# Optimization experiments

Hardware: AMD Instinct MI355X
Metric: run time of the kernel (lower is better)

Reference implementation:

```python
import jax, jax.numpy as jnp
import numpy as np

NUM_HEADS = 16
THETA = 10000.0


def apply_rope(x, pos, theta):
    # x: [B, H, S, d], pos: [S] int
    d = x.shape[-1]
    inv_freq = theta ** (-jnp.arange(0, d, 2, dtype=jnp.float32) / d)  # [d/2]
    ang = pos.astype(jnp.float32)[:, None] * inv_freq  # [S, d/2]
    cos, sin = jnp.cos(ang), jnp.sin(ang)
    x1, x2 = x[..., 0::2], x[..., 1::2]
    out_even = x1 * cos - x2 * sin
    out_odd = x1 * sin + x2 * cos
    return jnp.stack([out_even, out_odd], axis=-1).reshape(x.shape)


def setup_inputs() -> dict:
    key = jax.random.key(0)
    ks = jax.random.split(key, 5)
    B, S, D = 4, 2048, 2048
    s = 1.0 / np.sqrt(D)
    return {
        "x": jax.random.normal(ks[0], (B, S, D), dtype=jnp.float32),
        "token_positions": jnp.arange(S, dtype=jnp.int32),
        "wq": jax.random.normal(ks[1], (D, D), dtype=jnp.float32) * s,
        "wk": jax.random.normal(ks[2], (D, D), dtype=jnp.float32) * s,
        "wv": jax.random.normal(ks[3], (D, D), dtype=jnp.float32) * s,
        "wo": jax.random.normal(ks[4], (D, D), dtype=jnp.float32) * s,
    }


def reference(x, token_positions, wq, wk, wv, wo):
    B, S, _ = x.shape
    H = NUM_HEADS
    dh = wq.shape[0] // H

    def proj(w):
        y = jnp.einsum('bsd,ed->bse', x, w)  # Linear: x @ W^T
        return y.reshape(B, S, H, dh).transpose(0, 2, 1, 3)  # [B,H,S,dh]

    Q, K, V = proj(wq), proj(wk), proj(wv)
    Q = apply_rope(Q, token_positions, THETA)
    K = apply_rope(K, token_positions, THETA)

    scores = jnp.einsum('bhqd,bhkd->bhqk', Q, K) / jnp.sqrt(jnp.float32(dh))
    causal = jnp.tril(jnp.ones((S, S), dtype=bool))
    scores = jnp.where(causal, scores, jnp.finfo(scores.dtype).min)
    attn = jax.nn.softmax(scores, axis=-1)
    out = jnp.einsum('bhqk,bhkd->bhqd', attn, V)
    out = out.transpose(0, 2, 1, 3).reshape(B, S, H * dh)
    return jnp.einsum('bsd,ed->bse', out, wo)
```

## Files before the change

kernel.cpp:

```cpp
#include <hip/hip_runtime.h>
#include <math.h>

typedef __bf16 bf16;
typedef bf16 bf16x8 __attribute__((ext_vector_type(8)));
typedef bf16 bf16x4v __attribute__((ext_vector_type(4)));
typedef float f32x4 __attribute__((ext_vector_type(4)));

#define BB 4
#define SS 2048
#define DD 2048
#define HH 16
#define DH 128

__device__ __forceinline__ void gload_lds16(const bf16* g, bf16* l) {
  __builtin_amdgcn_global_load_lds(
      (const __attribute__((address_space(1))) void*)g,
      (__attribute__((address_space(3))) void*)l, 16, 0, 0);
}

__global__ __launch_bounds__(256) void cast_kernel(const float* __restrict__ in,
                                                   bf16* __restrict__ out, int n4) {
  int i = blockIdx.x * blockDim.x + threadIdx.x;
  if (i < n4) {
    const float4 v = ((const float4*)in)[i];
    bf16x4v o = {(bf16)v.x, (bf16)v.y, (bf16)v.z, (bf16)v.w};
    ((bf16x4v*)out)[i] = o;
  }
}

__global__ __launch_bounds__(256) void cast4_kernel(const float* __restrict__ w0,
                                                    const float* __restrict__ w1,
                                                    const float* __restrict__ w2,
                                                    const float* __restrict__ w3,
                                                    bf16* __restrict__ out) {
  const int i = blockIdx.x * blockDim.x + threadIdx.x;
  const int per = (DD * DD) / 4;
  const int sel = i / per, off = i - sel * per;
  const float* src = (sel == 0) ? w0 : (sel == 1) ? w1 : (sel == 2) ? w2 : w3;
  const float4 v = ((const float4*)src)[off];
  bf16x4v o = {(bf16)v.x, (bf16)v.y, (bf16)v.z, (bf16)v.w};
  ((bf16x4v*)(out + (size_t)sel * DD * DD))[off] = o;
}

template <int MODE>
__global__ __launch_bounds__(512, 2) void gemm256(const bf16* __restrict__ A,
                                                  const bf16* __restrict__ Bw,
                                                  bf16* __restrict__ Cb,
                                                  float* __restrict__ Cf,
                                                  const int* __restrict__ pos,
                                                  int M, int N, int K) {
  __shared__ alignas(16) bf16 lds[4][2][256 * 32];

  const int tid = threadIdx.x;
  const int wave = tid >> 6, lane = tid & 63;
  const int quad = lane >> 4, l15 = lane & 15;
  const int wm = wave >> 2, wn = wave & 3;

  const int lin = blockIdx.y * gridDim.x + blockIdx.x;
  const int swz = (lin & 7) * 32 + (lin >> 3);
  const int m0 = (swz >> 3) * 256, n0 = (swz & 7) * 256;

  auto stage = [&](int buf, int ab, const bf16* src, int rbase, int u) {
    bf16* dst = &lds[buf][ab][0];
#pragma unroll
    for (int j = 0; j < 2; ++j) {
      const int c = wave * 128 + j * 64 + lane;
      const int row = c >> 2;
      const int k8 = (c & 3) ^ ((row >> 1) & 3);
      gload_lds16(src + (size_t)(rbase + row) * K + u * 32 + k8 * 8,
                  dst + (size_t)(wave * 128 + j * 64) * 8);
    }
  };

  auto rdA = [&](int buf, int mf) -> bf16x8 {
    const int row = wm * 128 + mf * 16 + l15;
    return *(const bf16x8*)(&lds[buf][0][0] + row * 32 + ((quad ^ ((row >> 1) & 3)) * 8));
  };
  auto rdB = [&](int buf, int nf) -> bf16x8 {
    const int row = wn * 64 + nf * 16 + l15;
    return *(const bf16x8*)(&lds[buf][1][0] + row * 32 + ((quad ^ ((row >> 1) & 3)) * 8));
  };

  f32x4 acc[8][4] = {};
  const int NT = K >> 5;

  stage(0, 0, A, m0, 0);
  stage(0, 1, Bw, n0, 0);
  stage(1, 0, A, m0, 1);
  stage(1, 1, Bw, n0, 1);
  asm volatile("s_waitcnt vmcnt(4)" ::: "memory");
  __builtin_amdgcn_s_barrier();
  __builtin_amdgcn_sched_barrier(0);

  bf16x8 af[4], bfr[4];
  for (int t = 0; t < NT; ++t) {
    const int buf = t & 3;
    const bool pre = (t + 2 < NT);
#pragma unroll
    for (int mf = 0; mf < 4; ++mf) af[mf] = rdA(buf, mf);
#pragma unroll
    for (int nf = 0; nf < 4; ++nf) bfr[nf] = rdB(buf, nf);
    if (pre) stage((t + 2) & 3, 0, A, m0, t + 2);
    __builtin_amdgcn_sched_barrier(0);
    __builtin_amdgcn_s_barrier();
    asm volatile("s_waitcnt lgkmcnt(0)" ::: "memory");
    __builtin_amdgcn_sched_barrier(0);
    __builtin_amdgcn_s_setprio(1);
#pragma unroll
    for (int mf = 0; mf < 4; ++mf)
#pragma unroll
      for (int nf = 0; nf < 4; ++nf)
        acc[mf][nf] = __builtin_amdgcn_mfma_f32_16x16x32_bf16(af[mf], bfr[nf], acc[mf][nf], 0, 0, 0);
    __builtin_amdgcn_s_setprio(0);
    __builtin_amdgcn_sched_barrier(0);
    __builtin_amdgcn_s_barrier();
    __builtin_amdgcn_sched_barrier(0);
#pragma unroll
    for (int mf = 0; mf < 4; ++mf) af[mf] = rdA(buf, mf + 4);
    if (pre) stage((t + 2) & 3, 1, Bw, n0, t + 2);
    __builtin_amdgcn_sched_barrier(0);
    __builtin_amdgcn_s_barrier();
    asm volatile("s_waitcnt lgkmcnt(0)" ::: "memory");
    __builtin_amdgcn_sched_barrier(0);
    __builtin_amdgcn_s_setprio(1);
#pragma unroll
    for (int mf = 0; mf < 4; ++mf)
#pragma unroll
      for (int nf = 0; nf < 4; ++nf)
        acc[mf + 4][nf] = __builtin_amdgcn_mfma_f32_16x16x32_bf16(af[mf], bfr[nf], acc[mf + 4][nf], 0, 0, 0);
    __builtin_amdgcn_s_setprio(0);
    if (pre) asm volatile("s_waitcnt vmcnt(4)" ::: "memory");
    else     asm volatile("s_waitcnt vmcnt(0)" ::: "memory");
    __builtin_amdgcn_sched_barrier(0);
    __builtin_amdgcn_s_barrier();
    __builtin_amdgcn_sched_barrier(0);
  }

  float ps[8][4];
  if (MODE == 0) {
#pragma unroll
    for (int mf = 0; mf < 8; ++mf)
#pragma unroll
      for (int r = 0; r < 4; ++r)
        ps[mf][r] = (float)pos[(m0 + wm * 128 + mf * 16 + quad * 4 + r) & (SS - 1)];
  }

#pragma unroll
  for (int nf = 0; nf < 4; ++nf) {
    const int col = n0 + wn * 64 + nf * 16 + l15;
    float invf = 0.f, sgn = 0.f;
    if (MODE == 0) {
      const int d = col & (DH - 1);
      invf = exp2f((float)(d >> 1) * (-13.28771238f / 64.0f));
      sgn = (d & 1) ? 1.0f : -1.0f;
    }
#pragma unroll
    for (int mf = 0; mf < 8; ++mf) {
#pragma unroll
      for (int r = 0; r < 4; ++r) {
        const int row = m0 + wm * 128 + mf * 16 + quad * 4 + r;
        float v = acc[mf][nf][r];
        if (MODE == 0) {
          const float partner = __shfl_xor(v, 1);
          float sn, cn;
          __sincosf(ps[mf][r] * invf, &sn, &cn);
          v = fmaf(partner, sgn * sn, v * cn);
          const int b = row >> 11, s = row & (SS - 1);
          const int h = col >> 7, d = col & (DH - 1);
          Cb[((((size_t)b * HH + h) * SS + s) << 7) + d] = (bf16)v;
        } else if (MODE == 1) {
          const int b = row >> 11, s = row & (SS - 1);
          const int h = col >> 7, d = col & (DH - 1);
          Cb[(((size_t)b * HH + h) * DH + d) * SS + s] = (bf16)v;
        } else {
          Cf[(size_t)row * N + col] = v;
        }
      }
    }
  }
}

__global__ __launch_bounds__(256, 2) void flash_attn(const bf16* __restrict__ Q,
                                                     const bf16* __restrict__ Kg,
                                                     const bf16* __restrict__ Vt,
                                                     bf16* __restrict__ O) {
  __shared__ alignas(16) bf16 lK[2][64 * 128];
  __shared__ alignas(16) bf16 lP[4][32 * 64];

  const int tid = threadIdx.x;
  const int wave = tid >> 6, lane = tid & 63;
  const int quad = lane >> 4, l15 = lane & 15;
  const int swz = l15 & 7;

  const int lin = blockIdx.y * gridDim.x + blockIdx.x;
  const int bh = ((lin & 7) << 3) | ((lin >> 3) & 7);
  const int q0 = (15 - (lin >> 6)) * 128;

  const bf16* Qh = Q + (size_t)bh * SS * DH;
  const bf16* Kh = Kg + (size_t)bh * SS * DH;
  const bf16* Vh = Vt + (size_t)bh * DH * SS;
  const int nkb = (q0 >> 6) + 2;
  const int qrow0 = q0 + wave * 32;

  bf16x8 qf[2][4];
#pragma unroll
  for (int qt = 0; qt < 2; ++qt)
#pragma unroll
    for (int t = 0; t < 4; ++t)
      qf[qt][t] = *(const bf16x8*)(Qh + (size_t)(qrow0 + qt * 16 + l15) * DH + t * 32 + quad * 8);

  bf16* lPw = &lP[wave][0];
  const float cs = 0.12751649736f;
  const float MSTAT = 20.0f;
  float lsum[2] = {0.f, 0.f};
  f32x4 oacc[2][8] = {};
  int cur = 0;

  auto stage = [&](int b, int kb) {
#pragma unroll
    for (int j = 0; j < 4; ++j) {
      const int c = tid + j * 256;
      const int kr = c >> 4;
      gload_lds16(Kh + (size_t)(kb * 64 + kr) * DH + (((c & 15) ^ (kr & 7)) * 8),
                  &lK[b][0] + (size_t)(wave * 64 + j * 256) * 8);
    }
  };

  auto kv_iter = [&](int kb, bool masked) {
    int ktlim = 3;
    if (masked) {
      ktlim = (qrow0 + 31 - kb * 64) >> 4;
      if (ktlim < 0) return;
      if (ktlim > 3) ktlim = 3;
    }
    const bf16* kcur = &lK[cur][0];

    f32x4 sacc[2][4];
#pragma unroll
    for (int qt = 0; qt < 2; ++qt)
#pragma unroll
      for (int kt = 0; kt < 4; ++kt) sacc[qt][kt] = (f32x4){0.f, 0.f, 0.f, 0.f};
    __builtin_amdgcn_s_setprio(1);
#pragma unroll
    for (int kt = 0; kt < 4; ++kt) {
      if (kt <= ktlim) {
#pragma unroll
        for (int t = 0; t < 4; ++t) {
          const bf16x8 kfrag =
              *(const bf16x8*)(kcur + (kt * 16 + l15) * 128 + (((t * 4 + quad) ^ swz) * 8));
          sacc[0][kt] = __builtin_amdgcn_mfma_f32_16x16x32_bf16(kfrag, qf[0][t], sacc[0][kt], 0, 0, 0);
          sacc[1][kt] = __builtin_amdgcn_mfma_f32_16x16x32_bf16(kfrag, qf[1][t], sacc[1][kt], 0, 0, 0);
        }
      }
    }
    __builtin_amdgcn_s_setprio(0);

#pragma unroll
    for (int kt = 0; kt < 4; ++kt) {
#pragma unroll
      for (int qt = 0; qt < 2; ++qt) {
        bf16x4v pk = {(bf16)0.f, (bf16)0.f, (bf16)0.f, (bf16)0.f};
        if (kt <= ktlim) {
          float ls = 0.f;
#pragma unroll
          for (int r = 0; r < 4; ++r) {
            float e = exp2f(fmaf(sacc[qt][kt][r], cs, -MSTAT));
            if (masked) {
              const int key = kb * 64 + kt * 16 + quad * 4 + r;
              if (key > qrow0 + qt * 16 + l15) e = 0.f;
            }
            ls += e;
            pk[r] = (bf16)e;
          }
          lsum[qt] += ls;
        }
        *(bf16x4v*)(lPw + (qt * 16 + l15) * 64 + (((kt * 2 + (quad >> 1)) ^ swz) * 8) +
                    (quad & 1) * 4) = pk;
      }
    }

    bf16x8 pa[2][2];
#pragma unroll
    for (int qt = 0; qt < 2; ++qt)
#pragma unroll
      for (int kc = 0; kc < 2; ++kc)
        pa[qt][kc] = *(const bf16x8*)(lPw + (qt * 16 + l15) * 64 + (((kc * 4 + quad) ^ swz) * 8));

    __builtin_amdgcn_s_setprio(1);
#pragma unroll
    for (int g = 0; g < 2; ++g) {
      bf16x8 vf[4][2];
#pragma unroll
      for (int d2 = 0; d2 < 4; ++d2)
#pragma unroll
        for (int kc = 0; kc < 2; ++kc)
          vf[d2][kc] = *(const bf16x8*)(Vh + (size_t)((g * 4 + d2) * 16 + l15) * SS + kb * 64 +
                                        kc * 32 + quad * 8);
#pragma unroll
      for (int d2 = 0; d2 < 4; ++d2)
#pragma unroll
        for (int kc = 0; kc < 2; ++kc) {
          oacc[0][g * 4 + d2] =
              __builtin_amdgcn_mfma_f32_16x16x32_bf16(pa[0][kc], vf[d2][kc], oacc[0][g * 4 + d2], 0, 0, 0);
          oacc[1][g * 4 + d2] =
              __builtin_amdgcn_mfma_f32_16x16x32_bf16(pa[1][kc], vf[d2][kc], oacc[1][g * 4 + d2], 0, 0, 0);
        }
    }
    __builtin_amdgcn_s_setprio(0);
  };

  stage(0, 0);
  __syncthreads();

  for (int kb = 0; kb < nkb - 1; ++kb) {
    stage(cur ^ 1, kb + 1);
    kv_iter(kb, kb + 2 >= nkb);
    __syncthreads();
    cur ^= 1;
  }
  kv_iter(nkb - 1, true);

#pragma unroll
  for (int qt = 0; qt < 2; ++qt) {
    lsum[qt] += __shfl_xor(lsum[qt], 16);
    lsum[qt] += __shfl_xor(lsum[qt], 32);
  }

  const int b = bh >> 4, h = bh & 15;
#pragma unroll
  for (int qt = 0; qt < 2; ++qt) {
#pragma unroll
    for (int r = 0; r < 4; ++r) {
      const int qq = quad * 4 + r;
      const float il = 1.0f / __shfl(lsum[qt], qq);
      bf16* orow = O + ((size_t)b * SS + qrow0 + qt * 16 + qq) * DD + h * DH;
#pragma unroll
      for (int db = 0; db < 8; ++db) orow[db * 16 + l15] = (bf16)(oacc[qt][db][r] * il);
    }
  }
}

extern "C" void kernel_launch(void* const* d_in, const int* in_sizes, int n_in,
                              void* d_out, int out_size, void* d_ws, size_t ws_size,
                              hipStream_t stream) {
  (void)in_sizes; (void)n_in; (void)out_size; (void)ws_size;
  const float* x = (const float*)d_in[0];
  const int* pos = (const int*)d_in[1];
  const float* wq = (const float*)d_in[2];
  const float* wk = (const float*)d_in[3];
  const float* wv = (const float*)d_in[4];
  const float* wo = (const float*)d_in[5];
  float* out = (float*)d_out;

  bf16* xb  = (bf16*)d_ws;
  bf16* wqb = xb + (size_t)BB * SS * DD;
  bf16* wkb = wqb + (size_t)DD * DD;
  bf16* wvb = wkb + (size_t)DD * DD;
  bf16* wob = wvb + (size_t)DD * DD;
  bf16* Qb  = wob + (size_t)DD * DD;
  bf16* Kbf = Qb + (size_t)BB * SS * DD;
  bf16* Vtb = Kbf + (size_t)BB * SS * DD;
  bf16* Ob  = Vtb + (size_t)BB * SS * DD;

  const int nx = BB * SS * DD;
  cast_kernel<<<nx / 4 / 256, 256, 0, stream>>>(x, xb, nx / 4);
  cast4_kernel<<<DD * DD / 256, 256, 0, stream>>>(wq, wk, wv, wo, wqb);

  dim3 gg(DD / 256, (BB * SS) / 256);
  gemm256<0><<<gg, 512, 0, stream>>>(xb, wqb, Qb, nullptr, pos, BB * SS, DD, DD);
  gemm256<0><<<gg, 512, 0, stream>>>(xb, wkb, Kbf, nullptr, pos, BB * SS, DD, DD);
  gemm256<1><<<gg, 512, 0, stream>>>(xb, wvb, Vtb, nullptr, nullptr, BB * SS, DD, DD);

  flash_attn<<<dim3(SS / 128, BB * HH), 256, 0, stream>>>(Qb, Kbf, Vtb, Ob);

  gemm256<2><<<gg, 512, 0, stream>>>(Ob, wob, nullptr, out, nullptr, BB * SS, DD, DD);
}
```

Measured before the change: 636.6 us.

## Drop LDS K staging in flash attention, load K fragments directly from global

Removes the double-buffered LDS staging of K tiles and the per-iteration block barriers. Each wave now reads its K fragments straight from global memory, the same way V is already read. Launch bounds go from 2 to 4 blocks per SM to raise occupancy, since LDS use per block shrinks to just the P buffer. This trades shared K reuse across the four waves for redundant global/L2 traffic and exposed load latency. The higher occupancy is meant to hide that latency.

```diff
diff --git a/kernel.cpp b/kernel.cpp
--- a/kernel.cpp
+++ b/kernel.cpp
@@ -180,11 +180,10 @@
   }
 }
 
-__global__ __launch_bounds__(256, 2) void flash_attn(const bf16* __restrict__ Q,
+__global__ __launch_bounds__(256, 4) void flash_attn(const bf16* __restrict__ Q,
                                                      const bf16* __restrict__ Kg,
                                                      const bf16* __restrict__ Vt,
                                                      bf16* __restrict__ O) {
-  __shared__ alignas(16) bf16 lK[2][64 * 128];
   __shared__ alignas(16) bf16 lP[4][32 * 64];
 
   const int tid = threadIdx.x;
@@ -214,46 +213,38 @@
   const float MSTAT = 20.0f;
   float lsum[2] = {0.f, 0.f};
   f32x4 oacc[2][8] = {};
-  int cur = 0;
-
-  auto stage = [&](int b, int kb) {
-#pragma unroll
-    for (int j = 0; j < 4; ++j) {
-      const int c = tid + j * 256;
-      const int kr = c >> 4;
-      gload_lds16(Kh + (size_t)(kb * 64 + kr) * DH + (((c & 15) ^ (kr & 7)) * 8),
-                  &lK[b][0] + (size_t)(wave * 64 + j * 256) * 8);
-    }
-  };
-
-  auto kv_iter = [&](int kb, bool masked) {
+
+  for (int kb = 0; kb < nkb; ++kb) {
+    const bool masked = (kb + 2 >= nkb);
     int ktlim = 3;
     if (masked) {
       ktlim = (qrow0 + 31 - kb * 64) >> 4;
-      if (ktlim < 0) return;
+      if (ktlim < 0) continue;
       if (ktlim > 3) ktlim = 3;
     }
-    const bf16* kcur = &lK[cur][0];
+    const bf16* Kt = Kh + (size_t)(kb * 64) * DH;
 
     f32x4 sacc[2][4];
 #pragma unroll
     for (int qt = 0; qt < 2; ++qt)
 #pragma unroll
       for (int kt = 0; kt < 4; ++kt) sacc[qt][kt] = (f32x4){0.f, 0.f, 0.f, 0.f};
-    __builtin_amdgcn_s_setprio(1);
 #pragma unroll
     for (int kt = 0; kt < 4; ++kt) {
       if (kt <= ktlim) {
+        bf16x8 kf[4];
+#pragma unroll
+        for (int t = 0; t < 4; ++t)
+          kf[t] = *(const bf16x8*)(Kt + (size_t)(kt * 16 + l15) * DH + t * 32 + quad * 8);
+        __builtin_amdgcn_s_setprio(1);
 #pragma unroll
         for (int t = 0; t < 4; ++t) {
-          const bf16x8 kfrag =
-              *(const bf16x8*)(kcur + (kt * 16 + l15) * 128 + (((t * 4 + quad) ^ swz) * 8));
-          sacc[0][kt] = __builtin_amdgcn_mfma_f32_16x16x32_bf16(kfrag, qf[0][t], sacc[0][kt], 0, 0, 0);
-          sacc[1][kt] = __builtin_amdgcn_mfma_f32_16x16x32_bf16(kfrag, qf[1][t], sacc[1][kt], 0, 0, 0);
+          sacc[0][kt] = __builtin_amdgcn_mfma_f32_16x16x32_bf16(kf[t], qf[0][t], sacc[0][kt], 0, 0, 0);
+          sacc[1][kt] = __builtin_amdgcn_mfma_f32_16x16x32_bf16(kf[t], qf[1][t], sacc[1][kt], 0, 0, 0);
         }
+        __builtin_amdgcn_s_setprio(0);
       }
     }
-    __builtin_amdgcn_s_setprio(0);
 
 #pragma unroll
     for (int kt = 0; kt < 4; ++kt) {
@@ -286,7 +277,6 @@
       for (int kc = 0; kc < 2; ++kc)
         pa[qt][kc] = *(const bf16x8*)(lPw + (qt * 16 + l15) * 64 + (((kc * 4 + quad) ^ swz) * 8));
 
-    __builtin_amdgcn_s_setprio(1);
 #pragma unroll
     for (int g = 0; g < 2; ++g) {
       bf16x8 vf[4][2];
@@ -296,6 +286,7 @@
         for (int kc = 0; kc < 2; ++kc)
           vf[d2][kc] = *(const bf16x8*)(Vh + (size_t)((g * 4 + d2) * 16 + l15) * SS + kb * 64 +
                                         kc * 32 + quad * 8);
+      __builtin_amdgcn_s_setprio(1);
 #pragma unroll
       for (int d2 = 0; d2 < 4; ++d2)
 #pragma unroll
@@ -305,20 +296,9 @@
           oacc[1][g * 4 + d2] =
               __builtin_amdgcn_mfma_f32_16x16x32_bf16(pa[1][kc], vf[d2][kc], oacc[1][g * 4 + d2], 0, 0, 0);
         }
-    }
-    __builtin_amdgcn_s_setprio(0);
-  };
-
-  stage(0, 0);
-  __syncthreads();
-
-  for (int kb = 0; kb < nkb - 1; ++kb) {
-    stage(cur ^ 1, kb + 1);
-    kv_iter(kb, kb + 2 >= nkb);
-    __syncthreads();
-    cur ^= 1;
-  }
-  kv_iter(nkb - 1, true);
+      __builtin_amdgcn_s_setprio(0);
+    }
+  }
 
 #pragma unroll
   for (int qt = 0; qt < 2; ++qt) {
```

Result: slower. 970.3 us (+52.4%).

## Restructure GEMM main loop to BK=64 double buffering with quadrant-ordered MFMA

Applied to the files above, without the earlier changes.

Changes the GEMM k-tile from 32 to 64 with two LDS buffers instead of four, using a new 8-way XOR swizzle. Each iteration now issues the whole next tile's loads at once and splits compute into four quadrant phases, with fragment reloads interleaved between them. The aim is fewer loop iterations and barriers per unit of work. In exchange it waits for all loads (vmcnt(0)) at the end of each iteration, so prefetch depth drops to one tile and memory latency may be less hidden. It also re-reads A fragments from LDS more often.

```diff
diff --git a/kernel.cpp b/kernel.cpp
--- a/kernel.cpp
+++ b/kernel.cpp
@@ -49,7 +49,8 @@
                                                   float* __restrict__ Cf,
                                                   const int* __restrict__ pos,
                                                   int M, int N, int K) {
-  __shared__ alignas(16) bf16 lds[4][2][256 * 32];
+  __shared__ alignas(16) bf16 lA[2][256 * 64];
+  __shared__ alignas(16) bf16 lB[2][256 * 64];
 
   const int tid = threadIdx.x;
   const int wave = tid >> 6, lane = tid & 63;
@@ -60,47 +61,51 @@
   const int swz = (lin & 7) * 32 + (lin >> 3);
   const int m0 = (swz >> 3) * 256, n0 = (swz & 7) * 256;
 
-  auto stage = [&](int buf, int ab, const bf16* src, int rbase, int u) {
-    bf16* dst = &lds[buf][ab][0];
-#pragma unroll
-    for (int j = 0; j < 2; ++j) {
-      const int c = wave * 128 + j * 64 + lane;
-      const int row = c >> 2;
-      const int k8 = (c & 3) ^ ((row >> 1) & 3);
-      gload_lds16(src + (size_t)(rbase + row) * K + u * 32 + k8 * 8,
-                  dst + (size_t)(wave * 128 + j * 64) * 8);
+  auto stageT = [&](const bf16* src, bf16* dst, int rbase, int u) {
+#pragma unroll
+    for (int j = 0; j < 4; ++j) {
+      const int c = j * 512 + tid;
+      const int row = c >> 3, p = c & 7;
+      const int kc = p ^ (row & 7);
+      gload_lds16(src + (size_t)(rbase + row) * K + u * 64 + kc * 8,
+                  dst + (size_t)(j * 512 + wave * 64) * 8);
     }
   };
 
-  auto rdA = [&](int buf, int mf) -> bf16x8 {
+  auto rdA = [&](int buf, int mf, int kk) -> bf16x8 {
     const int row = wm * 128 + mf * 16 + l15;
-    return *(const bf16x8*)(&lds[buf][0][0] + row * 32 + ((quad ^ ((row >> 1) & 3)) * 8));
+    return *(const bf16x8*)(&lA[buf][0] + row * 64 + (((kk * 4 + quad) ^ (row & 7)) * 8));
   };
-  auto rdB = [&](int buf, int nf) -> bf16x8 {
+  auto rdB = [&](int buf, int nf, int kk) -> bf16x8 {
     const int row = wn * 64 + nf * 16 + l15;
-    return *(const bf16x8*)(&lds[buf][1][0] + row * 32 + ((quad ^ ((row >> 1) & 3)) * 8));
+    return *(const bf16x8*)(&lB[buf][0] + row * 64 + (((kk * 4 + quad) ^ (row & 7)) * 8));
   };
 
   f32x4 acc[8][4] = {};
-  const int NT = K >> 5;
-
-  stage(0, 0, A, m0, 0);
-  stage(0, 1, Bw, n0, 0);
-  stage(1, 0, A, m0, 1);
-  stage(1, 1, Bw, n0, 1);
-  asm volatile("s_waitcnt vmcnt(4)" ::: "memory");
+  const int NT = K >> 6;
+
+  stageT(A, &lA[0][0], m0, 0);
+  stageT(Bw, &lB[0][0], n0, 0);
+  asm volatile("s_waitcnt vmcnt(0)" ::: "memory");
   __builtin_amdgcn_s_barrier();
   __builtin_amdgcn_sched_barrier(0);
 
-  bf16x8 af[4], bfr[4];
+  bf16x8 af[4][2], bfr[2][2];
   for (int t = 0; t < NT; ++t) {
-    const int buf = t & 3;
-    const bool pre = (t + 2 < NT);
-#pragma unroll
-    for (int mf = 0; mf < 4; ++mf) af[mf] = rdA(buf, mf);
-#pragma unroll
-    for (int nf = 0; nf < 4; ++nf) bfr[nf] = rdB(buf, nf);
-    if (pre) stage((t + 2) & 3, 0, A, m0, t + 2);
+    const int buf = t & 1;
+
+#pragma unroll
+    for (int mf = 0; mf < 4; ++mf)
+#pragma unroll
+      for (int kk = 0; kk < 2; ++kk) af[mf][kk] = rdA(buf, mf, kk);
+#pragma unroll
+    for (int nf = 0; nf < 2; ++nf)
+#pragma unroll
+      for (int kk = 0; kk < 2; ++kk) bfr[nf][kk] = rdB(buf, nf, kk);
+    if (t + 1 < NT) {
+      stageT(A, &lA[buf ^ 1][0], m0, t + 1);
+      stageT(Bw, &lB[buf ^ 1][0], n0, t + 1);
+    }
     __builtin_amdgcn_sched_barrier(0);
     __builtin_amdgcn_s_barrier();
     asm volatile("s_waitcnt lgkmcnt(0)" ::: "memory");
@@ -109,15 +114,18 @@
 #pragma unroll
     for (int mf = 0; mf < 4; ++mf)
 #pragma unroll
-      for (int nf = 0; nf < 4; ++nf)
-        acc[mf][nf] = __builtin_amdgcn_mfma_f32_16x16x32_bf16(af[mf], bfr[nf], acc[mf][nf], 0, 0, 0);
-    __builtin_amdgcn_s_setprio(0);
-    __builtin_amdgcn_sched_barrier(0);
-    __builtin_amdgcn_s_barrier();
-    __builtin_amdgcn_sched_barrier(0);
-#pragma unroll
-    for (int mf = 0; mf < 4; ++mf) af[mf] = rdA(buf, mf + 4);
-    if (pre) stage((t + 2) & 3, 1, Bw, n0, t + 2);
+      for (int nf = 0; nf < 2; ++nf)
+#pragma unroll
+        for (int kk = 0; kk < 2; ++kk)
+          acc[mf][nf] = __builtin_amdgcn_mfma_f32_16x16x32_bf16(af[mf][kk], bfr[nf][kk], acc[mf][nf], 0, 0, 0);
+    __builtin_amdgcn_s_setprio(0);
+    __builtin_amdgcn_sched_barrier(0);
+    __builtin_amdgcn_s_barrier();
+
+#pragma unroll
+    for (int mf = 0; mf < 4; ++mf)
+#pragma unroll
+      for (int kk = 0; kk < 2; ++kk) af[mf][kk] = rdA(buf, mf + 4, kk);
     __builtin_amdgcn_sched_barrier(0);
     __builtin_amdgcn_s_barrier();
     asm volatile("s_waitcnt lgkmcnt(0)" ::: "memory");
@@ -126,11 +134,52 @@
 #pragma unroll
     for (int mf = 0; mf < 4; ++mf)
 #pragma unroll
-      for (int nf = 0; nf < 4; ++nf)
-        acc[mf + 4][nf] = __builtin_amdgcn_mfma_f32_16x16x32_bf16(af[mf], bfr[nf], acc[mf + 4][nf], 0, 0, 0);
-    __builtin_amdgcn_s_setprio(0);
-    if (pre) asm volatile("s_waitcnt vmcnt(4)" ::: "memory");
-    else     asm volatile("s_waitcnt vmcnt(0)" ::: "memory");
+      for (int nf = 0; nf < 2; ++nf)
+#pragma unroll
+        for (int kk = 0; kk < 2; ++kk)
+          acc[mf + 4][nf] = __builtin_amdgcn_mfma_f32_16x16x32_bf16(af[mf][kk], bfr[nf][kk], acc[mf + 4][nf], 0, 0, 0);
+    __builtin_amdgcn_s_setprio(0);
+    __builtin_amdgcn_sched_barrier(0);
+    __builtin_amdgcn_s_barrier();
+
+#pragma unroll
+    for (int nf = 0; nf < 2; ++nf)
+#pragma unroll
+      for (int kk = 0; kk < 2; ++kk) bfr[nf][kk] = rdB(buf, nf + 2, kk);
+    __builtin_amdgcn_sched_barrier(0);
+    __builtin_amdgcn_s_barrier();
+    asm volatile("s_waitcnt lgkmcnt(0)" ::: "memory");
+    __builtin_amdgcn_sched_barrier(0);
+    __builtin_amdgcn_s_setprio(1);
+#pragma unroll
+    for (int mf = 0; mf < 4; ++mf)
+#pragma unroll
+      for (int nf = 0; nf < 2; ++nf)
+#pragma unroll
+        for (int kk = 0; kk < 2; ++kk)
+          acc[mf + 4][nf + 2] = __builtin_amdgcn_mfma_f32_16x16x32_bf16(af[mf][kk], bfr[nf][kk], acc[mf + 4][nf + 2], 0, 0, 0);
+    __builtin_amdgcn_s_setprio(0);
+    __builtin_amdgcn_sched_barrier(0);
+    __builtin_amdgcn_s_barrier();
+
+#pragma unroll
+    for (int mf = 0; mf < 4; ++mf)
+#pragma unroll
+      for (int kk = 0; kk < 2; ++kk) af[mf][kk] = rdA(buf, mf, kk);
+    __builtin_amdgcn_sched_barrier(0);
+    __builtin_amdgcn_s_barrier();
+    asm volatile("s_waitcnt lgkmcnt(0)" ::: "memory");
+    __builtin_amdgcn_sched_barrier(0);
+    __builtin_amdgcn_s_setprio(1);
+#pragma unroll
+    for (int mf = 0; mf < 4; ++mf)
+#pragma unroll
+      for (int nf = 0; nf < 2; ++nf)
+#pragma unroll
+        for (int kk = 0; kk < 2; ++kk)
+          acc[mf][nf + 2] = __builtin_amdgcn_mfma_f32_16x16x32_bf16(af[mf][kk], bfr[nf][kk], acc[mf][nf + 2], 0, 0, 0);
+    __builtin_amdgcn_s_setprio(0);
+    asm volatile("s_waitcnt vmcnt(0)" ::: "memory");
     __builtin_amdgcn_sched_barrier(0);
     __builtin_amdgcn_s_barrier();
     __builtin_amdgcn_sched_barrier(0);
```

After: 646.7 us. No clear change (+1.6%).

## Restructure GEMM mainloop to BK=64 double-buffer with split A/B LDS halves

Applied to the files above, without the earlier changes.

Changes the 256x256 GEMM pipeline from a 4-deep ring of 32-wide K tiles to a double buffer of 64-wide K tiles. Each tile is split into two 32-wide halves held in separate A and B LDS arrays. The inner loop now loads all 8 A fragments and iterates over N fragments in pairs, which reduces barriers per K step and interleaves per-half prefetches of the next tile with MFMA work. The LDS swizzle changes from (row>>1)&3 to row&3. The new staging waits (vmcnt(4)) and the buffer reuse ordering are intricate, so there is a risk of races or of less latency hiding with only two buffers.

```diff
diff --git a/kernel.cpp b/kernel.cpp
--- a/kernel.cpp
+++ b/kernel.cpp
@@ -49,7 +49,8 @@
                                                   float* __restrict__ Cf,
                                                   const int* __restrict__ pos,
                                                   int M, int N, int K) {
-  __shared__ alignas(16) bf16 lds[4][2][256 * 32];
+  __shared__ alignas(16) bf16 lA[2][2][256 * 32];
+  __shared__ alignas(16) bf16 lB[2][2][256 * 32];
 
   const int tid = threadIdx.x;
   const int wave = tid >> 6, lane = tid & 63;
@@ -60,79 +61,104 @@
   const int swz = (lin & 7) * 32 + (lin >> 3);
   const int m0 = (swz >> 3) * 256, n0 = (swz & 7) * 256;
 
-  auto stage = [&](int buf, int ab, const bf16* src, int rbase, int u) {
-    bf16* dst = &lds[buf][ab][0];
+  auto stageH = [&](bf16* dst, const bf16* src, int rbase, int u, int kh) {
 #pragma unroll
     for (int j = 0; j < 2; ++j) {
-      const int c = wave * 128 + j * 64 + lane;
-      const int row = c >> 2;
-      const int k8 = (c & 3) ^ ((row >> 1) & 3);
-      gload_lds16(src + (size_t)(rbase + row) * K + u * 32 + k8 * 8,
-                  dst + (size_t)(wave * 128 + j * 64) * 8);
+      const int c = j * 512 + wave * 64 + lane;
+      const int row = c >> 2, p = c & 2 * 2 - 1;
+      const int kc = p ^ (row & 3);
+      gload_lds16(src + (size_t)(rbase + row) * K + u * 64 + kh * 32 + kc * 8,
+                  dst + (size_t)(j * 512 + wave * 64) * 8);
     }
   };
 
-  auto rdA = [&](int buf, int mf) -> bf16x8 {
+  auto rdA = [&](int buf, int kh, int mf) -> bf16x8 {
     const int row = wm * 128 + mf * 16 + l15;
-    return *(const bf16x8*)(&lds[buf][0][0] + row * 32 + ((quad ^ ((row >> 1) & 3)) * 8));
+    return *(const bf16x8*)(&lA[buf][kh][0] + row * 32 + ((quad ^ (row & 3)) * 8));
   };
-  auto rdB = [&](int buf, int nf) -> bf16x8 {
+  auto rdB = [&](int buf, int kh, int nf) -> bf16x8 {
     const int row = wn * 64 + nf * 16 + l15;
-    return *(const bf16x8*)(&lds[buf][1][0] + row * 32 + ((quad ^ ((row >> 1) & 3)) * 8));
+    return *(const bf16x8*)(&lB[buf][kh][0] + row * 32 + ((quad ^ (row & 3)) * 8));
   };
 
   f32x4 acc[8][4] = {};
-  const int NT = K >> 5;
-
-  stage(0, 0, A, m0, 0);
-  stage(0, 1, Bw, n0, 0);
-  stage(1, 0, A, m0, 1);
-  stage(1, 1, Bw, n0, 1);
-  asm volatile("s_waitcnt vmcnt(4)" ::: "memory");
-  __builtin_amdgcn_s_barrier();
-  __builtin_amdgcn_sched_barrier(0);
-
-  bf16x8 af[4], bfr[4];
+  const int NT = K >> 6;
+
+  stageH(&lA[0][0][0], A, m0, 0, 0);
+  stageH(&lB[0][0][0], Bw, n0, 0, 0);
+  stageH(&lA[0][1][0], A, m0, 0, 1);
+  stageH(&lB[0][1][0], Bw, n0, 0, 1);
+
+  bf16x8 af[8], bfr[2];
   for (int t = 0; t < NT; ++t) {
-    const int buf = t & 3;
-    const bool pre = (t + 2 < NT);
-#pragma unroll
-    for (int mf = 0; mf < 4; ++mf) af[mf] = rdA(buf, mf);
-#pragma unroll
-    for (int nf = 0; nf < 4; ++nf) bfr[nf] = rdB(buf, nf);
-    if (pre) stage((t + 2) & 3, 0, A, m0, t + 2);
-    __builtin_amdgcn_sched_barrier(0);
+    const int buf = t & 1;
+    const bool pre = (t + 1 < NT);
+
+    asm volatile("s_waitcnt vmcnt(4)" ::: "memory");
     __builtin_amdgcn_s_barrier();
+    __builtin_amdgcn_sched_barrier(0);
+#pragma unroll
+    for (int mf = 0; mf < 8; ++mf) af[mf] = rdA(buf, 0, mf);
+    bfr[0] = rdB(buf, 0, 0);
+    bfr[1] = rdB(buf, 0, 1);
+    if (pre) stageH(&lA[buf ^ 1][0][0], A, m0, t + 1, 0);
     asm volatile("s_waitcnt lgkmcnt(0)" ::: "memory");
     __builtin_amdgcn_sched_barrier(0);
     __builtin_amdgcn_s_setprio(1);
 #pragma unroll
-    for (int mf = 0; mf < 4; ++mf)
-#pragma unroll
-      for (int nf = 0; nf < 4; ++nf)
+    for (int mf = 0; mf < 8; ++mf)
+#pragma unroll
+      for (int nf = 0; nf < 2; ++nf)
         acc[mf][nf] = __builtin_amdgcn_mfma_f32_16x16x32_bf16(af[mf], bfr[nf], acc[mf][nf], 0, 0, 0);
     __builtin_amdgcn_s_setprio(0);
     __builtin_amdgcn_sched_barrier(0);
-    __builtin_amdgcn_s_barrier();
-    __builtin_amdgcn_sched_barrier(0);
-#pragma unroll
-    for (int mf = 0; mf < 4; ++mf) af[mf] = rdA(buf, mf + 4);
-    if (pre) stage((t + 2) & 3, 1, Bw, n0, t + 2);
-    __builtin_amdgcn_sched_barrier(0);
-    __builtin_amdgcn_s_barrier();
+
+    bfr[0] = rdB(buf, 0, 2);
+    bfr[1] = rdB(buf, 0, 3);
+    if (pre) stageH(&lB[buf ^ 1][0][0], Bw, n0, t + 1, 0);
     asm volatile("s_waitcnt lgkmcnt(0)" ::: "memory");
     __builtin_amdgcn_sched_barrier(0);
     __builtin_amdgcn_s_setprio(1);
 #pragma unroll
-    for (int mf = 0; mf < 4; ++mf)
-#pragma unroll
-      for (int nf = 0; nf < 4; ++nf)
-        acc[mf + 4][nf] = __builtin_amdgcn_mfma_f32_16x16x32_bf16(af[mf], bfr[nf], acc[mf + 4][nf], 0, 0, 0);
-    __builtin_amdgcn_s_setprio(0);
+    for (int mf = 0; mf < 8; ++mf)
+#pragma unroll
+      for (int nf = 0; nf < 2; ++nf)
+        acc[mf][nf + 2] = __builtin_amdgcn_mfma_f32_16x16x32_bf16(af[mf], bfr[nf], acc[mf][nf + 2], 0, 0, 0);
+    __builtin_amdgcn_s_setprio(0);
+    __builtin_amdgcn_sched_barrier(0);
+
     if (pre) asm volatile("s_waitcnt vmcnt(4)" ::: "memory");
     else     asm volatile("s_waitcnt vmcnt(0)" ::: "memory");
-    __builtin_amdgcn_sched_barrier(0);
     __builtin_amdgcn_s_barrier();
+    __builtin_amdgcn_sched_barrier(0);
+#pragma unroll
+    for (int mf = 0; mf < 8; ++mf) af[mf] = rdA(buf, 1, mf);
+    bfr[0] = rdB(buf, 1, 0);
+    bfr[1] = rdB(buf, 1, 1);
+    if (pre) stageH(&lA[buf ^ 1][1][0], A, m0, t + 1, 1);
+    asm volatile("s_waitcnt lgkmcnt(0)" ::: "memory");
+    __builtin_amdgcn_sched_barrier(0);
+    __builtin_amdgcn_s_setprio(1);
+#pragma unroll
+    for (int mf = 0; mf < 8; ++mf)
+#pragma unroll
+      for (int nf = 0; nf < 2; ++nf)
+        acc[mf][nf] = __builtin_amdgcn_mfma_f32_16x16x32_bf16(af[mf], bfr[nf], acc[mf][nf], 0, 0, 0);
+    __builtin_amdgcn_s_setprio(0);
+    __builtin_amdgcn_sched_barrier(0);
+
+    bfr[0] = rdB(buf, 1, 2);
+    bfr[1] = rdB(buf, 1, 3);
+    if (pre) stageH(&lB[buf ^ 1][1][0], Bw, n0, t + 1, 1);
+    asm volatile("s_waitcnt lgkmcnt(0)" ::: "memory");
+    __builtin_amdgcn_sched_barrier(0);
+    __builtin_amdgcn_s_setprio(1);
+#pragma unroll
+    for (int mf = 0; mf < 8; ++mf)
+#pragma unroll
+      for (int nf = 0; nf < 2; ++nf)
+        acc[mf][nf + 2] = __builtin_amdgcn_mfma_f32_16x16x32_bf16(af[mf], bfr[nf], acc[mf][nf + 2], 0, 0, 0);
+    __builtin_amdgcn_s_setprio(0);
     __builtin_amdgcn_sched_barrier(0);
   }
 
```

Measured after the change: 622.7 us. 2.2% less time.
